# Kernel tuning notes

Measured on AMD Instinct MI355X. Metric: run time of the kernel, lower is better.

## Reference

```python
import jax, jax.numpy as jnp
import numpy as np

N_NODES = 50000
N_EDGES = 800000
D_IN = 64
D_HID = 64
D_OUT = 64


def setup_inputs() -> dict:
    key = jax.random.key(0)
    ks = jax.random.split(key, 10)
    x = jax.random.normal(ks[0], (N_NODES, D_IN), dtype=jnp.float32)
    src = jax.random.randint(ks[1], (N_EDGES,), 0, N_NODES, dtype=jnp.int32)
    dst = jax.random.randint(ks[2], (N_EDGES,), 0, N_NODES, dtype=jnp.int32)
    s = 1.0 / np.sqrt(D_IN)
    W0 = jax.random.uniform(ks[3], (D_IN, D_HID), jnp.float32, -s, s)
    b0 = jnp.zeros((D_HID,), jnp.float32)
    W1 = jax.random.uniform(ks[4], (D_HID, D_HID), jnp.float32, -s, s)
    b1 = jnp.zeros((D_HID,), jnp.float32)
    W2 = jax.random.uniform(ks[5], (D_HID, D_OUT), jnp.float32, -s, s)
    b2 = jnp.zeros((D_OUT,), jnp.float32)
    return {"x": x, "src": src, "dst": dst, "W0": W0, "b0": b0,
            "W1": W1, "b1": b1, "W2": W2, "b2": b2}


def reference(x, src, dst, W0, b0, W1, b1, W2, b2):
    N = x.shape[0]
    # in-degree (constant across layers)
    deg = jax.ops.segment_sum(jnp.ones(src.shape[0], x.dtype), dst, num_segments=N)
    inv = (1.0 / (deg + 1.0))[:, None]  # [N,1] gcn normalizer (deg + self)

    def sage_gcn(h, W, b):
        # gather neighbor feats along edges, scatter-add to destinations
        agg = jax.ops.segment_sum(h[src], dst, num_segments=N)  # [N,d]
        h_neigh = (agg + h) * inv
        return h_neigh @ W + b

    h = sage_gcn(x, W0, b0)
    h = jax.nn.relu(h)
    h = sage_gcn(h, W1, b1)
    h = jax.nn.relu(h)
    h = sage_gcn(h, W2, b2)
    return h
```

## Files before the change

kernel.cpp:

```cpp
#include <hip/hip_runtime.h>
#include <hip/hip_fp16.h>

#define D 64

struct alignas(8) half4v { __half2 a, b; };

__global__ void count_deg_kernel(const int* __restrict__ dst, int* __restrict__ deg, int nE) {
    int e4 = (blockIdx.x * blockDim.x + threadIdx.x) * 4;
    if (e4 + 3 < nE) {
        int4 d = *(const int4*)(dst + e4);
        atomicAdd(&deg[d.x], 1);
        atomicAdd(&deg[d.y], 1);
        atomicAdd(&deg[d.z], 1);
        atomicAdd(&deg[d.w], 1);
    } else {
        for (int e = e4; e < nE; ++e) atomicAdd(&deg[dst[e]], 1);
    }
}

__global__ __launch_bounds__(256) void scan_a_kernel(const int* __restrict__ deg,
                                                     int* __restrict__ row_ptr,
                                                     int* __restrict__ blocksums, int N) {
    __shared__ int s[256];
    int t = threadIdx.x;
    int i = blockIdx.x * 256 + t;
    int v = (i < N) ? deg[i] : 0;
    s[t] = v;
    __syncthreads();
    #pragma unroll
    for (int d = 1; d < 256; d <<= 1) {
        int u = (t >= d) ? s[t - d] : 0;
        __syncthreads();
        s[t] += u;
        __syncthreads();
    }
    if (i < N) row_ptr[i] = s[t] - v;
    if (t == 255) blocksums[blockIdx.x] = s[255];
}

__global__ __launch_bounds__(256) void scan_b_kernel(int* __restrict__ blocksums,
                                                     int* __restrict__ row_ptr,
                                                     int nb, int N) {
    __shared__ int s[256];
    int t = threadIdx.x;
    int v = (t < nb) ? blocksums[t] : 0;
    s[t] = v;
    __syncthreads();
    #pragma unroll
    for (int d = 1; d < 256; d <<= 1) {
        int u = (t >= d) ? s[t - d] : 0;
        __syncthreads();
        s[t] += u;
        __syncthreads();
    }
    if (t < nb) blocksums[t] = s[t] - v;
    if (t == 255) row_ptr[N] = s[255];
}

__global__ __launch_bounds__(256) void scan_c_kernel(int* __restrict__ row_ptr,
                                                     int* __restrict__ cursor,
                                                     const int* __restrict__ blocksums, int N) {
    int i = blockIdx.x * 256 + threadIdx.x;
    if (i < N) {
        int r = row_ptr[i] + blocksums[blockIdx.x];
        row_ptr[i] = r;
        cursor[i] = r;
    }
}

__global__ __launch_bounds__(256) void fill_csr_sliced_kernel(
    const int* __restrict__ src, const int* __restrict__ dst,
    int* __restrict__ cursor, int* __restrict__ col,
    int nE, int slice_size)
{
    const int g  = blockIdx.x & 7;
    const int gb = blockIdx.x >> 3;
    const int lo = g * slice_size;
    const int hi = lo + slice_size;
    int e4 = (gb * 256 + (int)threadIdx.x) * 4;
    if (e4 + 3 < nE) {
        int4 d = *(const int4*)(dst + e4);
        bool m0 = (d.x >= lo) & (d.x < hi);
        bool m1 = (d.y >= lo) & (d.y < hi);
        bool m2 = (d.z >= lo) & (d.z < hi);
        bool m3 = (d.w >= lo) & (d.w < hi);
        if (m0 | m1 | m2 | m3) {
            int4 s = *(const int4*)(src + e4);
            if (m0) col[atomicAdd(&cursor[d.x], 1)] = s.x;
            if (m1) col[atomicAdd(&cursor[d.y], 1)] = s.y;
            if (m2) col[atomicAdd(&cursor[d.z], 1)] = s.z;
            if (m3) col[atomicAdd(&cursor[d.w], 1)] = s.w;
        }
    } else if (e4 < nE) {
        for (int e = e4; e < nE; ++e) {
            int dd = dst[e];
            if (dd >= lo && dd < hi) col[atomicAdd(&cursor[dd], 1)] = src[e];
        }
    }
}

template<bool IN_H, bool OUT_H>
__global__ __launch_bounds__(256, 4) void sage_layer_kernel(
    const void* __restrict__ hin, const int* __restrict__ row_ptr,
    const int* __restrict__ col, const float* __restrict__ W,
    const float* __restrict__ bias, void* __restrict__ hout,
    int N, int do_relu)
{
    __shared__ float Wlds[D * D];
    {
        const float4* W4 = (const float4*)W;
        float4* Wl4 = (float4*)Wlds;
        #pragma unroll
        for (int t = 0; t < 4; ++t)
            Wl4[t * 256 + threadIdx.x] = W4[t * 256 + threadIdx.x];
    }
    __syncthreads();

    const int lane = threadIdx.x & 63;
    const int sub  = lane >> 4;
    const int fq   = lane & 15;
    const int w    = threadIdx.x >> 6;
    const float bj = bias[lane];

    const float4*  __restrict__ hp4 = (const float4*)hin;
    const half4v* __restrict__ hph = (const half4v*)hin;

    const int nwaves = gridDim.x * 4;
    for (int i0 = blockIdx.x * 4 + w; i0 < N; i0 += nwaves) {
        const int i   = __builtin_amdgcn_readfirstlane(i0);
        const int rs  = __builtin_amdgcn_readfirstlane(row_ptr[i]);
        const int re  = __builtin_amdgcn_readfirstlane(row_ptr[i + 1]);
        const int deg = re - rs;

        float4 a0 = {0,0,0,0}, a1 = {0,0,0,0}, a2 = {0,0,0,0}, a3 = {0,0,0,0};
        int last_iv = 0;

        for (int e0 = rs; e0 < re; e0 += 64) {
            int ee = e0 + lane;
            int idxv = col[(ee < re) ? ee : (re - 1)];
            last_iv = idxv;
            int rem = re - e0;
            int steps = (((rem < 64) ? rem : 64) + 3) >> 2;
            int t = 0;
            for (; t + 4 <= steps; t += 4) {
                int base = (t << 2) + sub;
                int s0 = __shfl(idxv, base);
                int s1 = __shfl(idxv, base + 4);
                int s2 = __shfl(idxv, base + 8);
                int s3 = __shfl(idxv, base + 12);
                if constexpr (IN_H) {
                    half4v r0 = hph[(size_t)s0 * 16 + fq];
                    half4v r1 = hph[(size_t)s1 * 16 + fq];
                    half4v r2 = hph[(size_t)s2 * 16 + fq];
                    half4v r3 = hph[(size_t)s3 * 16 + fq];
                    float2 f;
                    f = __half22float2(r0.a); a0.x += f.x; a0.y += f.y;
                    f = __half22float2(r0.b); a0.z += f.x; a0.w += f.y;
                    f = __half22float2(r1.a); a1.x += f.x; a1.y += f.y;
                    f = __half22float2(r1.b); a1.z += f.x; a1.w += f.y;
                    f = __half22float2(r2.a); a2.x += f.x; a2.y += f.y;
                    f = __half22float2(r2.b); a2.z += f.x; a2.w += f.y;
                    f = __half22float2(r3.a); a3.x += f.x; a3.y += f.y;
                    f = __half22float2(r3.b); a3.z += f.x; a3.w += f.y;
                } else {
                    float4 v0 = hp4[(size_t)s0 * 16 + fq];
                    float4 v1 = hp4[(size_t)s1 * 16 + fq];
                    float4 v2 = hp4[(size_t)s2 * 16 + fq];
                    float4 v3 = hp4[(size_t)s3 * 16 + fq];
                    a0.x += v0.x; a0.y += v0.y; a0.z += v0.z; a0.w += v0.w;
                    a1.x += v1.x; a1.y += v1.y; a1.z += v1.z; a1.w += v1.w;
                    a2.x += v2.x; a2.y += v2.y; a2.z += v2.z; a2.w += v2.w;
                    a3.x += v3.x; a3.y += v3.y; a3.z += v3.z; a3.w += v3.w;
                }
            }
            for (; t < steps; ++t) {
                int s0 = __shfl(idxv, (t << 2) + sub);
                if constexpr (IN_H) {
                    half4v r0 = hph[(size_t)s0 * 16 + fq];
                    float2 f;
                    f = __half22float2(r0.a); a0.x += f.x; a0.y += f.y;
                    f = __half22float2(r0.b); a0.z += f.x; a0.w += f.y;
                } else {
                    float4 v0 = hp4[(size_t)s0 * 16 + fq];
                    a0.x += v0.x; a0.y += v0.y; a0.z += v0.z; a0.w += v0.w;
                }
            }
        }

        float4 tt;
        tt.x = (a0.x + a1.x) + (a2.x + a3.x);
        tt.y = (a0.y + a1.y) + (a2.y + a3.y);
        tt.z = (a0.z + a1.z) + (a2.z + a3.z);
        tt.w = (a0.w + a1.w) + (a2.w + a3.w);
        tt.x += __shfl_xor(tt.x, 16); tt.x += __shfl_xor(tt.x, 32);
        tt.y += __shfl_xor(tt.y, 16); tt.y += __shfl_xor(tt.y, 32);
        tt.z += __shfl_xor(tt.z, 16); tt.z += __shfl_xor(tt.z, 32);
        tt.w += __shfl_xor(tt.w, 16); tt.w += __shfl_xor(tt.w, 32);

        int pad = (-deg) & 3;
        if (deg > 0 && pad) {
            int last = __shfl(last_iv, 63);
            float4 vl;
            if constexpr (IN_H) {
                half4v rl = hph[(size_t)last * 16 + fq];
                float2 f0 = __half22float2(rl.a);
                float2 f1 = __half22float2(rl.b);
                vl = make_float4(f0.x, f0.y, f1.x, f1.y);
            } else {
                vl = hp4[(size_t)last * 16 + fq];
            }
            float fp = (float)pad;
            tt.x = fmaf(-fp, vl.x, tt.x);
            tt.y = fmaf(-fp, vl.y, tt.y);
            tt.z = fmaf(-fp, vl.z, tt.z);
            tt.w = fmaf(-fp, vl.w, tt.w);
        }

        float4 hs;
        if constexpr (IN_H) {
            half4v rs4 = hph[(size_t)i * 16 + fq];
            float2 f0 = __half22float2(rs4.a);
            float2 f1 = __half22float2(rs4.b);
            hs = make_float4(f0.x, f0.y, f1.x, f1.y);
        } else {
            hs = hp4[(size_t)i * 16 + fq];
        }
        float invd = 1.0f / (float)(deg + 1);
        tt.x = (tt.x + hs.x) * invd;
        tt.y = (tt.y + hs.y) * invd;
        tt.z = (tt.z + hs.z) * invd;
        tt.w = (tt.w + hs.w) * invd;

        float o0 = bj, o1 = 0.0f, o2 = 0.0f, o3 = 0.0f;
        #pragma unroll
        for (int k = 0; k < D; k += 4) {
            const int q = k >> 2;
            int t0 = __builtin_amdgcn_readlane(__float_as_int(tt.x), q);
            int t1 = __builtin_amdgcn_readlane(__float_as_int(tt.y), q);
            int t2 = __builtin_amdgcn_readlane(__float_as_int(tt.z), q);
            int t3 = __builtin_amdgcn_readlane(__float_as_int(tt.w), q);
            o0 = fmaf(__int_as_float(t0), Wlds[(k + 0) * D + lane], o0);
            o1 = fmaf(__int_as_float(t1), Wlds[(k + 1) * D + lane], o1);
            o2 = fmaf(__int_as_float(t2), Wlds[(k + 2) * D + lane], o2);
            o3 = fmaf(__int_as_float(t3), Wlds[(k + 3) * D + lane], o3);
        }
        float o = (o0 + o1) + (o2 + o3);
        if (do_relu) o = fmaxf(o, 0.0f);
        if constexpr (OUT_H) {
            ((__half*)hout)[(size_t)i * D + lane] = __float2half(o);
        } else {
            ((float*)hout)[(size_t)i * D + lane] = o;
        }
    }
}

extern "C" void kernel_launch(void* const* d_in, const int* in_sizes, int n_in,
                              void* d_out, int out_size, void* d_ws, size_t ws_size,
                              hipStream_t stream) {
    const float* x   = (const float*)d_in[0];
    const int*   src = (const int*)d_in[1];
    const int*   dst = (const int*)d_in[2];
    const float* W0  = (const float*)d_in[3];
    const float* b0  = (const float*)d_in[4];
    const float* W1  = (const float*)d_in[5];
    const float* b1  = (const float*)d_in[6];
    const float* W2  = (const float*)d_in[7];
    const float* b2  = (const float*)d_in[8];
    float* out = (float*)d_out;

    const int N = in_sizes[0] / D;
    const int E = in_sizes[1];

    const int scan_blocks = (N + 255) / 256;

    char* ws = (char*)d_ws;
    size_t off = 0;
    auto alloc = [&](size_t bytes) -> void* {
        void* p = ws + off;
        off = (off + bytes + 255) & ~(size_t)255;
        return p;
    };
    int*    deg       = (int*)   alloc((size_t)N * sizeof(int));
    int*    row_ptr   = (int*)   alloc((size_t)(N + 1) * sizeof(int));
    int*    cursor    = (int*)   alloc((size_t)N * sizeof(int));
    int*    blocksums = (int*)   alloc((size_t)scan_blocks * sizeof(int));
    int*    col       = (int*)   alloc((size_t)E * sizeof(int));
    __half* h1h       = (__half*)alloc((size_t)N * D * sizeof(__half));
    __half* h2h       = (__half*)alloc((size_t)N * D * sizeof(__half));

    hipMemsetAsync(deg, 0, (size_t)N * sizeof(int), stream);
    const int e4_blocks = (E / 4 + 255) / 256;
    count_deg_kernel<<<e4_blocks, 256, 0, stream>>>(dst, deg, E);
    scan_a_kernel<<<scan_blocks, 256, 0, stream>>>(deg, row_ptr, blocksums, N);
    scan_b_kernel<<<1, 256, 0, stream>>>(blocksums, row_ptr, scan_blocks, N);
    scan_c_kernel<<<scan_blocks, 256, 0, stream>>>(row_ptr, cursor, blocksums, N);
    const int slice_size = (N + 7) / 8;
    fill_csr_sliced_kernel<<<e4_blocks * 8, 256, 0, stream>>>(src, dst, cursor, col, E, slice_size);

    const int layer_blocks = 4096;

    sage_layer_kernel<false, true ><<<layer_blocks, 256, 0, stream>>>(x,   row_ptr, col, W0, b0, h1h, N, 1);
    sage_layer_kernel<true,  true ><<<layer_blocks, 256, 0, stream>>>(h1h, row_ptr, col, W1, b1, h2h, N, 1);
    sage_layer_kernel<true,  false><<<layer_blocks, 256, 0, stream>>>(h2h, row_ptr, col, W2, b2, out, N, 0);
}
```

Before: 284.1 us.

## Transform-then-aggregate: split each layer into fp16 GEMM and gather kernel

```diff
diff --git a/kernel.cpp b/kernel.cpp
--- a/kernel.cpp
+++ b/kernel.cpp
@@ -4,6 +4,12 @@
 #define D 64
 
 struct alignas(8) half4v { __half2 a, b; };
+typedef _Float16 h2_t __attribute__((ext_vector_type(2)));
+
+union v16u {
+    float4 f4;
+    h2_t   h2[4];
+};
 
 __global__ void count_deg_kernel(const int* __restrict__ dst, int* __restrict__ deg, int nE) {
     int e4 = (blockIdx.x * blockDim.x + threadIdx.x) * 4;
@@ -99,31 +105,65 @@
     }
 }
 
-template<bool IN_H, bool OUT_H>
-__global__ __launch_bounds__(256, 4) void sage_layer_kernel(
-    const void* __restrict__ hin, const int* __restrict__ row_ptr,
-    const int* __restrict__ col, const float* __restrict__ W,
-    const float* __restrict__ bias, void* __restrict__ hout,
-    int N, int do_relu)
+__global__ __launch_bounds__(256) void cvt_kernel(const float* __restrict__ x,
+                                                  __half* __restrict__ xh, int n) {
+    int stride = gridDim.x * 256 * 4;
+    for (int i = (blockIdx.x * 256 + threadIdx.x) * 4; i + 3 < n; i += stride) {
+        float4 v = *(const float4*)(x + i);
+        half4v o;
+        o.a = __floats2half2_rn(v.x, v.y);
+        o.b = __floats2half2_rn(v.z, v.w);
+        *(half4v*)(xh + i) = o;
+    }
+}
+
+__global__ __launch_bounds__(256) void gemm_kernel(
+    const __half* __restrict__ hin, const float* __restrict__ W,
+    __half* __restrict__ g, int N)
 {
-    __shared__ float Wlds[D * D];
-    {
-        const float4* W4 = (const float4*)W;
-        float4* Wl4 = (float4*)Wlds;
+    const int j   = threadIdx.x & 63;
+    const int wid = (blockIdx.x * blockDim.x + threadIdx.x) >> 6;
+    const int nw  = (gridDim.x * blockDim.x) >> 6;
+
+    h2_t wp[32];
+    #pragma unroll
+    for (int kk = 0; kk < 32; ++kk) {
+        h2_t p;
+        p[0] = (_Float16)W[(2 * kk + 0) * D + j];
+        p[1] = (_Float16)W[(2 * kk + 1) * D + j];
+        wp[kk] = p;
+    }
+
+    const float4* __restrict__ hin4 = (const float4*)hin;
+    for (int r = wid; r < N; r += nw) {
+        v16u buf[8];
         #pragma unroll
-        for (int t = 0; t < 4; ++t)
-            Wl4[t * 256 + threadIdx.x] = W4[t * 256 + threadIdx.x];
-    }
-    __syncthreads();
-
+        for (int t = 0; t < 8; ++t) buf[t].f4 = hin4[(size_t)r * 8 + t];
+        float o0 = 0.0f, o1 = 0.0f;
+        #pragma unroll
+        for (int t = 0; t < 8; ++t) {
+            o0 = __builtin_amdgcn_fdot2(buf[t].h2[0], wp[t * 4 + 0], o0, false);
+            o1 = __builtin_amdgcn_fdot2(buf[t].h2[1], wp[t * 4 + 1], o1, false);
+            o0 = __builtin_amdgcn_fdot2(buf[t].h2[2], wp[t * 4 + 2], o0, false);
+            o1 = __builtin_amdgcn_fdot2(buf[t].h2[3], wp[t * 4 + 3], o1, false);
+        }
+        g[(size_t)r * D + j] = __float2half(o0 + o1);
+    }
+}
+
+template<bool OUT_H>
+__global__ __launch_bounds__(256, 6) void agg_kernel(
+    const __half* __restrict__ g, const int* __restrict__ row_ptr,
+    const int* __restrict__ col, const float* __restrict__ bias,
+    void* __restrict__ hout, int N, int do_relu)
+{
     const int lane = threadIdx.x & 63;
     const int sub  = lane >> 4;
     const int fq   = lane & 15;
     const int w    = threadIdx.x >> 6;
-    const float bj = bias[lane];
-
-    const float4*  __restrict__ hp4 = (const float4*)hin;
-    const half4v* __restrict__ hph = (const half4v*)hin;
+    const float4 b4 = ((const float4*)bias)[fq];
+
+    const half4v* __restrict__ gh = (const half4v*)g;
 
     const int nwaves = gridDim.x * 4;
     for (int i0 = blockIdx.x * 4 + w; i0 < N; i0 += nwaves) {
@@ -148,42 +188,26 @@
                 int s1 = __shfl(idxv, base + 4);
                 int s2 = __shfl(idxv, base + 8);
                 int s3 = __shfl(idxv, base + 12);
-                if constexpr (IN_H) {
-                    half4v r0 = hph[(size_t)s0 * 16 + fq];
-                    half4v r1 = hph[(size_t)s1 * 16 + fq];
-                    half4v r2 = hph[(size_t)s2 * 16 + fq];
-                    half4v r3 = hph[(size_t)s3 * 16 + fq];
-                    float2 f;
-                    f = __half22float2(r0.a); a0.x += f.x; a0.y += f.y;
-                    f = __half22float2(r0.b); a0.z += f.x; a0.w += f.y;
-                    f = __half22float2(r1.a); a1.x += f.x; a1.y += f.y;
-                    f = __half22float2(r1.b); a1.z += f.x; a1.w += f.y;
-                    f = __half22float2(r2.a); a2.x += f.x; a2.y += f.y;
-                    f = __half22float2(r2.b); a2.z += f.x; a2.w += f.y;
-                    f = __half22float2(r3.a); a3.x += f.x; a3.y += f.y;
-                    f = __half22float2(r3.b); a3.z += f.x; a3.w += f.y;
-                } else {
-                    float4 v0 = hp4[(size_t)s0 * 16 + fq];
-                    float4 v1 = hp4[(size_t)s1 * 16 + fq];
-                    float4 v2 = hp4[(size_t)s2 * 16 + fq];
-                    float4 v3 = hp4[(size_t)s3 * 16 + fq];
-                    a0.x += v0.x; a0.y += v0.y; a0.z += v0.z; a0.w += v0.w;
-                    a1.x += v1.x; a1.y += v1.y; a1.z += v1.z; a1.w += v1.w;
-                    a2.x += v2.x; a2.y += v2.y; a2.z += v2.z; a2.w += v2.w;
-                    a3.x += v3.x; a3.y += v3.y; a3.z += v3.z; a3.w += v3.w;
-                }
+                half4v r0 = gh[(size_t)s0 * 16 + fq];
+                half4v r1 = gh[(size_t)s1 * 16 + fq];
+                half4v r2 = gh[(size_t)s2 * 16 + fq];
+                half4v r3 = gh[(size_t)s3 * 16 + fq];
+                float2 f;
+                f = __half22float2(r0.a); a0.x += f.x; a0.y += f.y;
+                f = __half22float2(r0.b); a0.z += f.x; a0.w += f.y;
+                f = __half22float2(r1.a); a1.x += f.x; a1.y += f.y;
+                f = __half22float2(r1.b); a1.z += f.x; a1.w += f.y;
+                f = __half22float2(r2.a); a2.x += f.x; a2.y += f.y;
+                f = __half22float2(r2.b); a2.z += f.x; a2.w += f.y;
+                f = __half22float2(r3.a); a3.x += f.x; a3.y += f.y;
+                f = __half22float2(r3.b); a3.z += f.x; a3.w += f.y;
             }
             for (; t < steps; ++t) {
                 int s0 = __shfl(idxv, (t << 2) + sub);
-                if constexpr (IN_H) {
-                    half4v r0 = hph[(size_t)s0 * 16 + fq];
-                    float2 f;
-                    f = __half22float2(r0.a); a0.x += f.x; a0.y += f.y;
-                    f = __half22float2(r0.b); a0.z += f.x; a0.w += f.y;
-                } else {
-                    float4 v0 = hp4[(size_t)s0 * 16 + fq];
-                    a0.x += v0.x; a0.y += v0.y; a0.z += v0.z; a0.w += v0.w;
-                }
+                half4v r0 = gh[(size_t)s0 * 16 + fq];
+                float2 f;
+                f = __half22float2(r0.a); a0.x += f.x; a0.y += f.y;
+                f = __half22float2(r0.b); a0.z += f.x; a0.w += f.y;
             }
         }
 
@@ -200,56 +224,38 @@
         int pad = (-deg) & 3;
         if (deg > 0 && pad) {
             int last = __shfl(last_iv, 63);
-            float4 vl;
-            if constexpr (IN_H) {
-                half4v rl = hph[(size_t)last * 16 + fq];
-                float2 f0 = __half22float2(rl.a);
-                float2 f1 = __half22float2(rl.b);
-                vl = make_float4(f0.x, f0.y, f1.x, f1.y);
+            half4v rl = gh[(size_t)last * 16 + fq];
+            float2 f0 = __half22float2(rl.a);
+            float2 f1 = __half22float2(rl.b);
+            float fp = (float)pad;
+            tt.x = fmaf(-fp, f0.x, tt.x);
+            tt.y = fmaf(-fp, f0.y, tt.y);
+            tt.z = fmaf(-fp, f1.x, tt.z);
+            tt.w = fmaf(-fp, f1.y, tt.w);
+        }
+
+        half4v rs4 = gh[(size_t)i * 16 + fq];
+        float2 s0f = __half22float2(rs4.a);
+        float2 s1f = __half22float2(rs4.b);
+        float invd = 1.0f / (float)(deg + 1);
+        float ox = fmaf(tt.x + s0f.x, invd, b4.x);
+        float oy = fmaf(tt.y + s0f.y, invd, b4.y);
+        float oz = fmaf(tt.z + s1f.x, invd, b4.z);
+        float ow = fmaf(tt.w + s1f.y, invd, b4.w);
+        if (do_relu) {
+            ox = fmaxf(ox, 0.0f); oy = fmaxf(oy, 0.0f);
+            oz = fmaxf(oz, 0.0f); ow = fmaxf(ow, 0.0f);
+        }
+        if (sub == 0) {
+            if constexpr (OUT_H) {
+                half4v o;
+                o.a = __floats2half2_rn(ox, oy);
+                o.b = __floats2half2_rn(oz, ow);
+                ((half4v*)hout)[(size_t)i * 16 + fq] = o;
             } else {
-                vl = hp4[(size_t)last * 16 + fq];
+                float4 o = make_float4(ox, oy, oz, ow);
+                ((float4*)hout)[(size_t)i * 16 + fq] = o;
             }
-            float fp = (float)pad;
-            tt.x = fmaf(-fp, vl.x, tt.x);
-            tt.y = fmaf(-fp, vl.y, tt.y);
-            tt.z = fmaf(-fp, vl.z, tt.z);
-            tt.w = fmaf(-fp, vl.w, tt.w);
-        }
-
-        float4 hs;
-        if constexpr (IN_H) {
-            half4v rs4 = hph[(size_t)i * 16 + fq];
-            float2 f0 = __half22float2(rs4.a);
-            float2 f1 = __half22float2(rs4.b);
-            hs = make_float4(f0.x, f0.y, f1.x, f1.y);
-        } else {
-            hs = hp4[(size_t)i * 16 + fq];
-        }
-        float invd = 1.0f / (float)(deg + 1);
-        tt.x = (tt.x + hs.x) * invd;
-        tt.y = (tt.y + hs.y) * invd;
-        tt.z = (tt.z + hs.z) * invd;
-        tt.w = (tt.w + hs.w) * invd;
-
-        float o0 = bj, o1 = 0.0f, o2 = 0.0f, o3 = 0.0f;
-        #pragma unroll
-        for (int k = 0; k < D; k += 4) {
-            const int q = k >> 2;
-            int t0 = __builtin_amdgcn_readlane(__float_as_int(tt.x), q);
-            int t1 = __builtin_amdgcn_readlane(__float_as_int(tt.y), q);
-            int t2 = __builtin_amdgcn_readlane(__float_as_int(tt.z), q);
-            int t3 = __builtin_amdgcn_readlane(__float_as_int(tt.w), q);
-            o0 = fmaf(__int_as_float(t0), Wlds[(k + 0) * D + lane], o0);
-            o1 = fmaf(__int_as_float(t1), Wlds[(k + 1) * D + lane], o1);
-            o2 = fmaf(__int_as_float(t2), Wlds[(k + 2) * D + lane], o2);
-            o3 = fmaf(__int_as_float(t3), Wlds[(k + 3) * D + lane], o3);
-        }
-        float o = (o0 + o1) + (o2 + o3);
-        if (do_relu) o = fmaxf(o, 0.0f);
-        if constexpr (OUT_H) {
-            ((__half*)hout)[(size_t)i * D + lane] = __float2half(o);
-        } else {
-            ((float*)hout)[(size_t)i * D + lane] = o;
         }
     }
 }
@@ -285,8 +291,10 @@
     int*    cursor    = (int*)   alloc((size_t)N * sizeof(int));
     int*    blocksums = (int*)   alloc((size_t)scan_blocks * sizeof(int));
     int*    col       = (int*)   alloc((size_t)E * sizeof(int));
-    __half* h1h       = (__half*)alloc((size_t)N * D * sizeof(__half));
-    __half* h2h       = (__half*)alloc((size_t)N * D * sizeof(__half));
+    __half* xh        = (__half*)alloc((size_t)N * D * sizeof(__half));
+    __half* gbuf      = (__half*)alloc((size_t)N * D * sizeof(__half));
+    __half* h1        = (__half*)alloc((size_t)N * D * sizeof(__half));
+    __half* h2        = (__half*)alloc((size_t)N * D * sizeof(__half));
 
     hipMemsetAsync(deg, 0, (size_t)N * sizeof(int), stream);
     const int e4_blocks = (E / 4 + 255) / 256;
@@ -297,9 +305,15 @@
     const int slice_size = (N + 7) / 8;
     fill_csr_sliced_kernel<<<e4_blocks * 8, 256, 0, stream>>>(src, dst, cursor, col, E, slice_size);
 
-    const int layer_blocks = 4096;
-
-    sage_layer_kernel<false, true ><<<layer_blocks, 256, 0, stream>>>(x,   row_ptr, col, W0, b0, h1h, N, 1);
-    sage_layer_kernel<true,  true ><<<layer_blocks, 256, 0, stream>>>(h1h, row_ptr, col, W1, b1, h2h, N, 1);
-    sage_layer_kernel<true,  false><<<layer_blocks, 256, 0, stream>>>(h2h, row_ptr, col, W2, b2, out, N, 0);
-}
+    cvt_kernel<<<1024, 256, 0, stream>>>(x, xh, N * D);
+
+    const int gemm_blocks = 1024;
+    const int agg_blocks  = 4096;
+
+    gemm_kernel<<<gemm_blocks, 256, 0, stream>>>(xh, W0, gbuf, N);
+    agg_kernel<true ><<<agg_blocks, 256, 0, stream>>>(gbuf, row_ptr, col, b0, h1,  N, 1);
+    gemm_kernel<<<gemm_blocks, 256, 0, stream>>>(h1, W1, gbuf, N);
+    agg_kernel<true ><<<agg_blocks, 256, 0, stream>>>(gbuf, row_ptr, col, b1, h2,  N, 1);
+    gemm_kernel<<<gemm_blocks, 256, 0, stream>>>(h2, W2, gbuf, N);
+    agg_kernel<false><<<agg_blocks, 256, 0, stream>>>(gbuf, row_ptr, col, b2, out, N, 0);
+}
```

Result: no change. 285.4 us (+0.5%).
